# Performance work log

Hardware: AMD Instinct MI355X
Metric: run time of the kernel (lower is better)

## Reference

```python
import jax, jax.numpy as jnp
import numpy as np

LN_EPS = 1e-5   # nn.LayerNorm default eps
EPS = 1e-3      # norm epsilon in module

B, R, S, C, CO, OUT = 1, 256, 128, 256, 32, 128  # res, seq, c_m, outer_channel, output_channel


def setup_inputs() -> dict:
    key = jax.random.key(0)
    ks = jax.random.split(key, 6)
    act = jax.random.normal(ks[0], (B, R, S, C), jnp.float32)
    mask = jnp.ones((B, S, R), jnp.float32)
    ln_gamma = jnp.ones((C,), jnp.float32)
    ln_beta = jnp.zeros((C,), jnp.float32)
    w_left = jax.random.normal(ks[1], (CO, C), jnp.float32) * (1.0 / np.sqrt(C))
    b_left = jnp.zeros((CO,), jnp.float32)
    w_right = jax.random.normal(ks[2], (CO, C), jnp.float32) * (1.0 / np.sqrt(C))
    b_right = jnp.zeros((CO,), jnp.float32)
    w_o = jax.random.normal(ks[3], (OUT, CO * CO), jnp.float32) * (1.0 / np.sqrt(CO * CO))
    b_o = jnp.zeros((OUT,), jnp.float32)
    return {"act": act, "mask": mask, "ln_gamma": ln_gamma, "ln_beta": ln_beta,
            "w_left": w_left, "b_left": b_left, "w_right": w_right, "b_right": b_right,
            "w_o": w_o, "b_o": b_o}


def reference(act, mask, ln_gamma, ln_beta, w_left, b_left, w_right, b_right, w_o, b_o):
    # act: [B, R(res), S(seq), C]; mask: [B, S, R]
    x = jnp.swapaxes(act, -3, -2)                     # permute_final_dims (1,0,2) -> [B, S, R, C]
    mu = x.mean(-1, keepdims=True)
    var = x.var(-1, keepdims=True)
    xn = (x - mu) * jax.lax.rsqrt(var + LN_EPS) * ln_gamma + ln_beta
    m = mask[..., None]                               # [B, S, R, 1]
    left = m * (xn @ w_left.T + b_left)               # [B, S, R, CO]
    right = m * (xn @ w_right.T + b_right)            # [B, S, R, CO]
    # outer product mean over seq dim: out[b,i,j,c,d] = sum_s left[b,s,i,c] * right[b,s,j,d]
    op = jnp.einsum('bsic,bsjd->bijcd', left, right)  # [B, R, R, CO, CO]
    op = op.reshape(op.shape[:3] + (CO * CO,))        # flatten_final_dims(.., 2)
    out = op @ w_o.T + b_o                            # [B, R, R, OUT]
    norm = jnp.einsum('bsi,bsj->bij', mask, mask)[..., None]  # [B, R, R, 1]
    return out / (EPS + norm)
```

## Files before the change

### kernel.cpp

```cpp
#include <hip/hip_runtime.h>
#include <hip/hip_bf16.h>
#include <stdint.h>

#define R_ 256
#define S_ 128
#define C_ 256
#define CO_ 32
#define OUT_ 128
#define LN_EPS 1e-5f
#define EPS_ 1e-3f

typedef __attribute__((ext_vector_type(8))) short bf16x8;
typedef __attribute__((ext_vector_type(4))) float f32x4;

static __device__ __forceinline__ unsigned short f2bf(float f) {
  union { float f; uint32_t u; } cv; cv.f = f;
  uint32_t u = cv.u;
  uint32_t r = (u + 0x7FFFu + ((u >> 16) & 1u)) >> 16;
  return (unsigned short)r;
}

__global__ void k_prep_w(const float* wl, const float* wr, const float* gamma,
                         const float* beta, const float* bl, const float* br,
                         unsigned short* wcat, float* g1, float* g0, float* bcat) {
  int co = blockIdx.x;
  int c = threadIdx.x;
  const float* src = (co < 32) ? (wl + co * C_) : (wr + (co - 32) * C_);
  float w = src[c], g = gamma[c], bt = beta[c];
  float wg = w * g;
  wcat[co * C_ + c] = f2bf(wg);
  __shared__ float red1[256], red0[256];
  red1[c] = wg; red0[c] = w * bt;
  __syncthreads();
  for (int off = 128; off > 0; off >>= 1) {
    if (c < off) { red1[c] += red1[c + off]; red0[c] += red0[c + off]; }
    __syncthreads();
  }
  if (c == 0) {
    g1[co] = red1[0];
    g0[co] = red0[0];
    bcat[co] = (co < 32) ? bl[co] : br[co - 32];
  }
}

__global__ void k_cast_wo(const float* wo, unsigned short* wob) {
  int t = blockIdx.x * 256 + threadIdx.x;
  float4 v = ((const float4*)wo)[t];
  ushort4 o;
  o.x = f2bf(v.x); o.y = f2bf(v.y); o.z = f2bf(v.z); o.w = f2bf(v.w);
  ((ushort4*)wob)[t] = o;
}

__global__ void k_norm(const float* mask, float* invn) {
  int i = blockIdx.x, j = threadIdx.x;
  float a = 0.f;
  for (int s = 0; s < S_; ++s) a += mask[s * R_ + i] * mask[s * R_ + j];
  invn[i * R_ + j] = 1.0f / (EPS_ + a);
}

#define AP 264
__global__ __launch_bounds__(256) void k_proj(
    const float* act, const float* mask, const unsigned short* wcat,
    const float* g1v, const float* g0v, const float* bcv,
    unsigned short* leftg, unsigned short* rightg) {
  __shared__ unsigned short a_bf[S_ * AP];
  __shared__ unsigned short w_l[64 * AP];
  __shared__ float mu_s[S_], rs_s[S_], mk_s[S_];
  __shared__ float g1s[64], g0s[64], bcs[64];
  int tid = threadIdx.x;
  int r = blockIdx.x;

  const float4* actv = (const float4*)(act + (size_t)r * (S_ * C_));
  for (int it = 0; it < 32; ++it) {
    int f = tid + it * 256;
    int s = f >> 6;
    int c4 = (f & 63) * 4;
    float4 v = actv[f];
    ushort4 o;
    o.x = f2bf(v.x); o.y = f2bf(v.y); o.z = f2bf(v.z); o.w = f2bf(v.w);
    *(ushort4*)&a_bf[s * AP + c4] = o;
  }
  const uint4* wsrc = (const uint4*)wcat;
  for (int it = 0; it < 8; ++it) {
    int f = tid + it * 256;
    int co = f >> 5, ch = f & 31;
    *(uint4*)&w_l[co * AP + ch * 8] = wsrc[f];
  }
  if (tid < 128) mk_s[tid] = mask[tid * R_ + r];
  if (tid < 64) { g1s[tid] = g1v[tid]; g0s[tid] = g0v[tid]; bcs[tid] = bcv[tid]; }
  __syncthreads();

  if (tid < 128) {
    float sum = 0.f, sq = 0.f;
    for (int i = 0; i < 32; ++i) {
      uint4 v = *(const uint4*)&a_bf[tid * AP + i * 8];
      uint32_t ws_[4] = {v.x, v.y, v.z, v.w};
#pragma unroll
      for (int q = 0; q < 4; ++q) {
        union { uint32_t u; float f; } lo, hi;
        lo.u = ws_[q] << 16;
        hi.u = ws_[q] & 0xFFFF0000u;
        sum += lo.f + hi.f;
        sq += lo.f * lo.f + hi.f * hi.f;
      }
    }
    float mu = sum * (1.0f / C_);
    float var = sq * (1.0f / C_) - mu * mu;
    mu_s[tid] = mu;
    rs_s[tid] = rsqrtf(var + LN_EPS);
  }
  __syncthreads();

  int lane = tid & 63, wid = tid >> 6;
  int l15 = lane & 15, l4 = lane >> 4;
  f32x4 acc[2][4];
#pragma unroll
  for (int a = 0; a < 2; ++a)
#pragma unroll
    for (int b = 0; b < 4; ++b) acc[a][b] = (f32x4){0.f, 0.f, 0.f, 0.f};
  for (int ks = 0; ks < 8; ++ks) {
    bf16x8 af[2], bfr[4];
#pragma unroll
    for (int mf = 0; mf < 2; ++mf) {
      int row = wid * 32 + mf * 16 + l15;
      af[mf] = *(const bf16x8*)&a_bf[row * AP + ks * 32 + l4 * 8];
    }
#pragma unroll
    for (int nf = 0; nf < 4; ++nf) {
      int row = nf * 16 + l15;
      bfr[nf] = *(const bf16x8*)&w_l[row * AP + ks * 32 + l4 * 8];
    }
#pragma unroll
    for (int mf = 0; mf < 2; ++mf)
#pragma unroll
      for (int nf = 0; nf < 4; ++nf)
        acc[mf][nf] = __builtin_amdgcn_mfma_f32_16x16x32_bf16(af[mf], bfr[nf], acc[mf][nf], 0, 0, 0);
  }
  __syncthreads();

  unsigned short* trans = w_l;
#pragma unroll
  for (int mf = 0; mf < 2; ++mf) {
#pragma unroll
    for (int nf = 0; nf < 4; ++nf) {
      int co = nf * 16 + l15;
      float G1 = g1s[co], G0 = g0s[co], BC = bcs[co];
#pragma unroll
      for (int reg = 0; reg < 4; ++reg) {
        int s = wid * 32 + mf * 16 + l4 * 4 + reg;
        float v = rs_s[s] * acc[mf][nf][reg] - mu_s[s] * rs_s[s] * G1 + G0 + BC;
        v *= mk_s[s];
        trans[co * 136 + s] = f2bf(v);
      }
    }
  }
  __syncthreads();

  uint4* lg = (uint4*)leftg;
  uint4* rg = (uint4*)rightg;
  for (int it = 0; it < 4; ++it) {
    int idx = tid + it * 256;
    int row = idx >> 4, ch = idx & 15;
    uint4 val = *(const uint4*)&trans[row * 136 + ch * 8];
    if (row < 32) lg[((size_t)r * 32 + row) * 16 + ch] = val;
    else          rg[((size_t)r * 32 + (row - 32)) * 16 + ch] = val;
  }
}

#define SROW 136
#define OPROW 1032
__global__ __launch_bounds__(512, 2) void k_main(
    const unsigned short* __restrict__ leftg, const unsigned short* __restrict__ rightg,
    const unsigned short* __restrict__ wob, const float* __restrict__ bo,
    const float* __restrict__ invn, float* __restrict__ out) {
  __shared__ __align__(16) unsigned char sm[2 * 256 * 272];
  unsigned short* sa = (unsigned short*)sm;
  unsigned short* sb = (unsigned short*)(sm + 256 * 272);
  unsigned short* opb = (unsigned short*)sm;
  int tid = threadIdx.x;
  int bi = blockIdx.x >> 5, bj = blockIdx.x & 31;

  const uint4* lsrc = (const uint4*)leftg + (size_t)bi * 256 * 16;
  const uint4* rsrc = (const uint4*)rightg + (size_t)bj * 256 * 16;
  for (int it = 0; it < 8; ++it) {
    int idx = tid + it * 512;
    int row = idx >> 4, ch = idx & 15;
    *(uint4*)&sa[row * SROW + ch * 8] = lsrc[idx];
    *(uint4*)&sb[row * SROW + ch * 8] = rsrc[idx];
  }
  __syncthreads();

  int lane = tid & 63, w = tid >> 6;
  int l15 = lane & 15, l4 = lane >> 4;

  int wm = w >> 2, wn = w & 3;
  f32x4 acc[8][4];
#pragma unroll
  for (int a = 0; a < 8; ++a)
#pragma unroll
    for (int b = 0; b < 4; ++b) acc[a][b] = (f32x4){0.f, 0.f, 0.f, 0.f};
  for (int ks = 0; ks < 4; ++ks) {
    bf16x8 af[8], bfr[4];
#pragma unroll
    for (int mf = 0; mf < 8; ++mf)
      af[mf] = *(const bf16x8*)&sa[(wm * 128 + mf * 16 + l15) * SROW + ks * 32 + l4 * 8];
#pragma unroll
    for (int nf = 0; nf < 4; ++nf)
      bfr[nf] = *(const bf16x8*)&sb[(wn * 64 + nf * 16 + l15) * SROW + ks * 32 + l4 * 8];
#pragma unroll
    for (int mf = 0; mf < 8; ++mf)
#pragma unroll
      for (int nf = 0; nf < 4; ++nf)
        acc[mf][nf] = __builtin_amdgcn_mfma_f32_16x16x32_bf16(af[mf], bfr[nf], acc[mf][nf], 0, 0, 0);
  }
  __syncthreads();

#pragma unroll
  for (int mf = 0; mf < 8; ++mf) {
    int mbase = wm * 128 + mf * 16 + l4 * 4;
#pragma unroll
    for (int nf = 0; nf < 4; ++nf) {
      int n = wn * 64 + nf * 16 + l15;
      int j = n >> 5, d = n & 31;
#pragma unroll
      for (int reg = 0; reg < 4; ++reg) {
        int m = mbase + reg;
        int i = m >> 5, c = m & 31;
        opb[(i * 8 + j) * OPROW + c * 32 + d] = f2bf(acc[mf][nf][reg]);
      }
    }
  }
  __syncthreads();

  int o = w * 16 + l15;
  f32x4 acc2[4];
#pragma unroll
  for (int a = 0; a < 4; ++a) acc2[a] = (f32x4){0.f, 0.f, 0.f, 0.f};
  const uint4* wrow = (const uint4*)(wob + (size_t)o * 1024);
  uint4 bnext = wrow[l4];
  for (int ks2 = 0; ks2 < 32; ++ks2) {
    uint4 bcur = bnext;
    if (ks2 < 31) bnext = wrow[(ks2 + 1) * 4 + l4];
    bf16x8 b2 = *(const bf16x8*)&bcur;
    bf16x8 a2[4];
#pragma unroll
    for (int mf = 0; mf < 4; ++mf)
      a2[mf] = *(const bf16x8*)&opb[(mf * 16 + l15) * OPROW + ks2 * 32 + l4 * 8];
#pragma unroll
    for (int mf = 0; mf < 4; ++mf)
      acc2[mf] = __builtin_amdgcn_mfma_f32_16x16x32_bf16(a2[mf], b2, acc2[mf], 0, 0, 0);
  }

  float bov = bo[o];
#pragma unroll
  for (int mf = 0; mf < 4; ++mf) {
#pragma unroll
    for (int reg = 0; reg < 4; ++reg) {
      int p = mf * 16 + l4 * 4 + reg;
      int gi = bi * 8 + (p >> 3), gj = bj * 8 + (p & 7);
      float v = (acc2[mf][reg] + bov) * invn[gi * R_ + gj];
      out[((size_t)(gi * R_ + gj)) * OUT_ + o] = v;
    }
  }
}

extern "C" void kernel_launch(void* const* d_in, const int* in_sizes, int n_in,
                              void* d_out, int out_size, void* d_ws, size_t ws_size,
                              hipStream_t stream) {
  (void)in_sizes; (void)n_in; (void)out_size; (void)ws_size;
  const float* act   = (const float*)d_in[0];
  const float* mask  = (const float*)d_in[1];
  const float* gamma = (const float*)d_in[2];
  const float* beta  = (const float*)d_in[3];
  const float* wl    = (const float*)d_in[4];
  const float* bl    = (const float*)d_in[5];
  const float* wr    = (const float*)d_in[6];
  const float* br    = (const float*)d_in[7];
  const float* wo    = (const float*)d_in[8];
  const float* bo    = (const float*)d_in[9];
  float* out = (float*)d_out;
  unsigned char* ws = (unsigned char*)d_ws;
  unsigned short* leftg  = (unsigned short*)(ws + 0);
  unsigned short* rightg = (unsigned short*)(ws + 2097152);
  unsigned short* wob    = (unsigned short*)(ws + 4194304);
  float* invn            = (float*)(ws + 4456448);
  unsigned short* wcat   = (unsigned short*)(ws + 4718592);
  float* g1              = (float*)(ws + 4751360);
  float* g0              = (float*)(ws + 4751616);
  float* bcat            = (float*)(ws + 4751872);

  hipLaunchKernelGGL(k_prep_w, dim3(64), dim3(256), 0, stream,
                     wl, wr, gamma, beta, bl, br, wcat, g1, g0, bcat);
  hipLaunchKernelGGL(k_cast_wo, dim3(128), dim3(256), 0, stream, wo, wob);
  hipLaunchKernelGGL(k_norm, dim3(256), dim3(256), 0, stream, mask, invn);
  hipLaunchKernelGGL(k_proj, dim3(256), dim3(256), 0, stream,
                     act, mask, wcat, g1, g0, bcat, leftg, rightg);
  hipLaunchKernelGGL(k_main, dim3(1024), dim3(512), 0, stream,
                     leftg, rightg, wob, bo, invn, out);
}
```

Baseline: 173.1 us.

## Merge prep kernels, split projection over seq halves, swizzle LDS and split-K output GEMM

Fuses the three weight/norm prep kernels into one launch and pre-permutes w_o into an MFMA-friendly tiled layout. The projection kernel now runs two blocks per residue, each covering half the sequence, and computes LayerNorm statistics in fp32 with wave shuffles while loading. The main kernel loads left/right tiles straight into XOR-swizzled LDS with global_load_lds and writes the outer-product buffer swizzled to avoid bank conflicts. The output GEMM is split over K across two wave groups and reduced through LDS. These changes target launch overhead, LDS bank conflicts and load latency, at the cost of an extra reduction pass and more complex indexing.

```diff
diff --git a/kernel.cpp b/kernel.cpp
--- a/kernel.cpp
+++ b/kernel.cpp
@@ -12,6 +12,8 @@
 
 typedef __attribute__((ext_vector_type(8))) short bf16x8;
 typedef __attribute__((ext_vector_type(4))) float f32x4;
+typedef __attribute__((address_space(1))) const unsigned int GAS;
+typedef __attribute__((address_space(3))) unsigned int LAS;
 
 static __device__ __forceinline__ unsigned short f2bf(float f) {
   union { float f; uint32_t u; } cv; cv.f = f;
@@ -20,178 +22,162 @@
   return (unsigned short)r;
 }
 
-__global__ void k_prep_w(const float* wl, const float* wr, const float* gamma,
-                         const float* beta, const float* bl, const float* br,
-                         unsigned short* wcat, float* g1, float* g0, float* bcat) {
-  int co = blockIdx.x;
-  int c = threadIdx.x;
-  const float* src = (co < 32) ? (wl + co * C_) : (wr + (co - 32) * C_);
-  float w = src[c], g = gamma[c], bt = beta[c];
-  float wg = w * g;
-  wcat[co * C_ + c] = f2bf(wg);
-  __shared__ float red1[256], red0[256];
-  red1[c] = wg; red0[c] = w * bt;
-  __syncthreads();
-  for (int off = 128; off > 0; off >>= 1) {
-    if (c < off) { red1[c] += red1[c + off]; red0[c] += red0[c + off]; }
+__global__ __launch_bounds__(256) void k_prep(
+    const float* wl, const float* wr, const float* gamma, const float* beta,
+    const float* bl, const float* br, const float* wo, const float* mask,
+    unsigned short* wcat, float* g1, float* g0, float* bcat,
+    unsigned short* wob2, float* invn) {
+  int bid = blockIdx.x, tid = threadIdx.x;
+  if (bid < 64) {
+    int co = bid, c = tid;
+    const float* src = (co < 32) ? (wl + co * C_) : (wr + (co - 32) * C_);
+    float w = src[c], g = gamma[c], bt = beta[c];
+    float wg = w * g;
+    wcat[co * C_ + c] = f2bf(wg);
+    __shared__ float red1[256], red0[256];
+    red1[c] = wg; red0[c] = w * bt;
     __syncthreads();
-  }
-  if (c == 0) {
-    g1[co] = red1[0];
-    g0[co] = red0[0];
-    bcat[co] = (co < 32) ? bl[co] : br[co - 32];
-  }
-}
-
-__global__ void k_cast_wo(const float* wo, unsigned short* wob) {
-  int t = blockIdx.x * 256 + threadIdx.x;
-  float4 v = ((const float4*)wo)[t];
-  ushort4 o;
-  o.x = f2bf(v.x); o.y = f2bf(v.y); o.z = f2bf(v.z); o.w = f2bf(v.w);
-  ((ushort4*)wob)[t] = o;
-}
-
-__global__ void k_norm(const float* mask, float* invn) {
-  int i = blockIdx.x, j = threadIdx.x;
-  float a = 0.f;
-  for (int s = 0; s < S_; ++s) a += mask[s * R_ + i] * mask[s * R_ + j];
-  invn[i * R_ + j] = 1.0f / (EPS_ + a);
-}
-
-#define AP 264
-__global__ __launch_bounds__(256) void k_proj(
-    const float* act, const float* mask, const unsigned short* wcat,
-    const float* g1v, const float* g0v, const float* bcv,
-    unsigned short* leftg, unsigned short* rightg) {
-  __shared__ unsigned short a_bf[S_ * AP];
-  __shared__ unsigned short w_l[64 * AP];
-  __shared__ float mu_s[S_], rs_s[S_], mk_s[S_];
+    for (int off = 128; off > 0; off >>= 1) {
+      if (c < off) { red1[c] += red1[c + off]; red0[c] += red0[c + off]; }
+      __syncthreads();
+    }
+    if (c == 0) {
+      g1[co] = red1[0]; g0[co] = red0[0];
+      bcat[co] = (co < 32) ? bl[co] : br[co - 32];
+    }
+  } else if (bid < 192) {
+    int o = bid - 64;
+    float4 v = ((const float4*)wo)[o * 256 + tid];
+    float vv[4] = {v.x, v.y, v.z, v.w};
+#pragma unroll
+    for (int e = 0; e < 4; ++e) {
+      int kk = tid * 4 + e;
+      int kk2 = (kk & 31) * 32 + (kk >> 5);
+      wob2[(kk2 >> 3) * 1024 + o * 8 + (kk2 & 7)] = f2bf(vv[e]);
+    }
+  } else {
+    int i = bid - 192, j = tid;
+    float a = 0.f;
+    for (int s = 0; s < S_; ++s) a += mask[s * R_ + i] * mask[s * R_ + j];
+    invn[i * R_ + j] = 1.0f / (EPS_ + a);
+  }
+}
+
+#define AP2 264
+__global__ __launch_bounds__(256, 2) void k_proj(
+    const float* __restrict__ act, const float* __restrict__ mask,
+    const unsigned short* __restrict__ wcat,
+    const float* __restrict__ g1v, const float* __restrict__ g0v,
+    const float* __restrict__ bcv,
+    unsigned short* __restrict__ leftg, unsigned short* __restrict__ rightg) {
+  __shared__ __align__(16) unsigned short a_bf[64 * AP2];
+  __shared__ __align__(16) unsigned short w_l[64 * AP2];
+  __shared__ __align__(16) unsigned short trans[64 * 72];
+  __shared__ float mu_s[64], rs_s[64], mk_s[64];
   __shared__ float g1s[64], g0s[64], bcs[64];
   int tid = threadIdx.x;
-  int r = blockIdx.x;
-
-  const float4* actv = (const float4*)(act + (size_t)r * (S_ * C_));
-  for (int it = 0; it < 32; ++it) {
-    int f = tid + it * 256;
-    int s = f >> 6;
-    int c4 = (f & 63) * 4;
-    float4 v = actv[f];
+  int lane = tid & 63, w = tid >> 6;
+  int r = blockIdx.x >> 1;
+  int sh = (blockIdx.x & 1) * 64;
+
+  const float4* actv = (const float4*)act;
+  for (int it = 0; it < 16; ++it) {
+    int s = w + it * 4;
+    float4 v = actv[(size_t)r * 8192 + (size_t)(sh + s) * 64 + lane];
+    float ls = v.x + v.y + v.z + v.w;
+    float lq = v.x * v.x + v.y * v.y + v.z * v.z + v.w * v.w;
+#pragma unroll
+    for (int off = 32; off > 0; off >>= 1) {
+      ls += __shfl_xor(ls, off);
+      lq += __shfl_xor(lq, off);
+    }
+    if (lane == 0) {
+      float mu = ls * (1.0f / 256.0f);
+      float var = lq * (1.0f / 256.0f) - mu * mu;
+      mu_s[s] = mu;
+      rs_s[s] = rsqrtf(var + LN_EPS);
+    }
     ushort4 o;
     o.x = f2bf(v.x); o.y = f2bf(v.y); o.z = f2bf(v.z); o.w = f2bf(v.w);
-    *(ushort4*)&a_bf[s * AP + c4] = o;
+    *(ushort4*)&a_bf[s * AP2 + lane * 4] = o;
   }
   const uint4* wsrc = (const uint4*)wcat;
   for (int it = 0; it < 8; ++it) {
     int f = tid + it * 256;
     int co = f >> 5, ch = f & 31;
-    *(uint4*)&w_l[co * AP + ch * 8] = wsrc[f];
-  }
-  if (tid < 128) mk_s[tid] = mask[tid * R_ + r];
-  if (tid < 64) { g1s[tid] = g1v[tid]; g0s[tid] = g0v[tid]; bcs[tid] = bcv[tid]; }
-  __syncthreads();
-
-  if (tid < 128) {
-    float sum = 0.f, sq = 0.f;
-    for (int i = 0; i < 32; ++i) {
-      uint4 v = *(const uint4*)&a_bf[tid * AP + i * 8];
-      uint32_t ws_[4] = {v.x, v.y, v.z, v.w};
-#pragma unroll
-      for (int q = 0; q < 4; ++q) {
-        union { uint32_t u; float f; } lo, hi;
-        lo.u = ws_[q] << 16;
-        hi.u = ws_[q] & 0xFFFF0000u;
-        sum += lo.f + hi.f;
-        sq += lo.f * lo.f + hi.f * hi.f;
-      }
-    }
-    float mu = sum * (1.0f / C_);
-    float var = sq * (1.0f / C_) - mu * mu;
-    mu_s[tid] = mu;
-    rs_s[tid] = rsqrtf(var + LN_EPS);
-  }
-  __syncthreads();
-
-  int lane = tid & 63, wid = tid >> 6;
+    *(uint4*)&w_l[co * AP2 + ch * 8] = wsrc[f];
+  }
+  if (tid < 64) {
+    mk_s[tid] = mask[(size_t)(sh + tid) * R_ + r];
+    g1s[tid] = g1v[tid]; g0s[tid] = g0v[tid]; bcs[tid] = bcv[tid];
+  }
+  __syncthreads();
+
   int l15 = lane & 15, l4 = lane >> 4;
-  f32x4 acc[2][4];
-#pragma unroll
-  for (int a = 0; a < 2; ++a)
-#pragma unroll
-    for (int b = 0; b < 4; ++b) acc[a][b] = (f32x4){0.f, 0.f, 0.f, 0.f};
+  f32x4 acc[4];
+#pragma unroll
+  for (int b = 0; b < 4; ++b) acc[b] = (f32x4){0.f, 0.f, 0.f, 0.f};
   for (int ks = 0; ks < 8; ++ks) {
-    bf16x8 af[2], bfr[4];
-#pragma unroll
-    for (int mf = 0; mf < 2; ++mf) {
-      int row = wid * 32 + mf * 16 + l15;
-      af[mf] = *(const bf16x8*)&a_bf[row * AP + ks * 32 + l4 * 8];
-    }
+    bf16x8 af = *(const bf16x8*)&a_bf[(w * 16 + l15) * AP2 + ks * 32 + l4 * 8];
 #pragma unroll
     for (int nf = 0; nf < 4; ++nf) {
-      int row = nf * 16 + l15;
-      bfr[nf] = *(const bf16x8*)&w_l[row * AP + ks * 32 + l4 * 8];
-    }
-#pragma unroll
-    for (int mf = 0; mf < 2; ++mf)
-#pragma unroll
-      for (int nf = 0; nf < 4; ++nf)
-        acc[mf][nf] = __builtin_amdgcn_mfma_f32_16x16x32_bf16(af[mf], bfr[nf], acc[mf][nf], 0, 0, 0);
-  }
-  __syncthreads();
-
-  unsigned short* trans = w_l;
-#pragma unroll
-  for (int mf = 0; mf < 2; ++mf) {
-#pragma unroll
-    for (int nf = 0; nf < 4; ++nf) {
-      int co = nf * 16 + l15;
-      float G1 = g1s[co], G0 = g0s[co], BC = bcs[co];
-#pragma unroll
-      for (int reg = 0; reg < 4; ++reg) {
-        int s = wid * 32 + mf * 16 + l4 * 4 + reg;
-        float v = rs_s[s] * acc[mf][nf][reg] - mu_s[s] * rs_s[s] * G1 + G0 + BC;
-        v *= mk_s[s];
-        trans[co * 136 + s] = f2bf(v);
-      }
-    }
-  }
-  __syncthreads();
-
-  uint4* lg = (uint4*)leftg;
-  uint4* rg = (uint4*)rightg;
-  for (int it = 0; it < 4; ++it) {
-    int idx = tid + it * 256;
-    int row = idx >> 4, ch = idx & 15;
-    uint4 val = *(const uint4*)&trans[row * 136 + ch * 8];
-    if (row < 32) lg[((size_t)r * 32 + row) * 16 + ch] = val;
-    else          rg[((size_t)r * 32 + (row - 32)) * 16 + ch] = val;
-  }
-}
-
-#define SROW 136
-#define OPROW 1032
+      bf16x8 bfr = *(const bf16x8*)&w_l[(nf * 16 + l15) * AP2 + ks * 32 + l4 * 8];
+      acc[nf] = __builtin_amdgcn_mfma_f32_16x16x32_bf16(af, bfr, acc[nf], 0, 0, 0);
+    }
+  }
+#pragma unroll
+  for (int nf = 0; nf < 4; ++nf) {
+    int co = nf * 16 + l15;
+    float G1 = g1s[co], G0 = g0s[co], BC = bcs[co];
+#pragma unroll
+    for (int reg = 0; reg < 4; ++reg) {
+      int s = w * 16 + l4 * 4 + reg;
+      float v = rs_s[s] * acc[nf][reg] - mu_s[s] * rs_s[s] * G1 + G0 + BC;
+      v *= mk_s[s];
+      trans[co * 72 + s] = f2bf(v);
+    }
+  }
+  __syncthreads();
+
+  for (int it2 = 0; it2 < 2; ++it2) {
+    int idx = tid + it2 * 256;
+    int row = idx >> 3, ch = idx & 7;
+    uint4 val = *(const uint4*)&trans[row * 72 + ch * 8];
+    if (row < 32)
+      ((uint4*)leftg)[((size_t)(r * 32 + row)) * 16 + (sh >> 3) + ch] = val;
+    else
+      ((uint4*)rightg)[((size_t)(r * 32 + row - 32)) * 16 + (sh >> 3) + ch] = val;
+  }
+}
+
 __global__ __launch_bounds__(512, 2) void k_main(
     const unsigned short* __restrict__ leftg, const unsigned short* __restrict__ rightg,
-    const unsigned short* __restrict__ wob, const float* __restrict__ bo,
+    const unsigned short* __restrict__ wob2, const float* __restrict__ bo,
     const float* __restrict__ invn, float* __restrict__ out) {
-  __shared__ __align__(16) unsigned char sm[2 * 256 * 272];
-  unsigned short* sa = (unsigned short*)sm;
-  unsigned short* sb = (unsigned short*)(sm + 256 * 272);
-  unsigned short* opb = (unsigned short*)sm;
+  __shared__ __align__(16) unsigned char smem[131072];
+  unsigned char* opbytes = smem;
+  unsigned short* opu16 = (unsigned short*)smem;
+  float* redf = (float*)smem;
   int tid = threadIdx.x;
-  int bi = blockIdx.x >> 5, bj = blockIdx.x & 31;
-
-  const uint4* lsrc = (const uint4*)leftg + (size_t)bi * 256 * 16;
-  const uint4* rsrc = (const uint4*)rightg + (size_t)bj * 256 * 16;
-  for (int it = 0; it < 8; ++it) {
-    int idx = tid + it * 512;
-    int row = idx >> 4, ch = idx & 15;
-    *(uint4*)&sa[row * SROW + ch * 8] = lsrc[idx];
-    *(uint4*)&sb[row * SROW + ch * 8] = rsrc[idx];
-  }
-  __syncthreads();
-
   int lane = tid & 63, w = tid >> 6;
   int l15 = lane & 15, l4 = lane >> 4;
+  int bi = blockIdx.x >> 5, bj = blockIdx.x & 31;
+
+  {
+    const unsigned char* gA = (const unsigned char*)leftg + (size_t)bi * 65536;
+    const unsigned char* gB = (const unsigned char*)rightg + (size_t)bj * 65536;
+#pragma unroll
+    for (int k = 0; k < 8; ++k) {
+      int rowbase = w * 32 + k * 4;
+      int row = rowbase + (lane >> 4);
+      int ch = (lane & 15) ^ (row & 7);
+      __builtin_amdgcn_global_load_lds((GAS*)(gA + row * 256 + ch * 16),
+                                       (LAS*)&smem[rowbase * 256], 16, 0, 0);
+      __builtin_amdgcn_global_load_lds((GAS*)(gB + row * 256 + ch * 16),
+                                       (LAS*)&smem[65536 + rowbase * 256], 16, 0, 0);
+    }
+  }
+  __syncthreads();
 
   int wm = w >> 2, wn = w & 3;
   f32x4 acc[8][4];
@@ -202,11 +188,17 @@
   for (int ks = 0; ks < 4; ++ks) {
     bf16x8 af[8], bfr[4];
 #pragma unroll
-    for (int mf = 0; mf < 8; ++mf)
-      af[mf] = *(const bf16x8*)&sa[(wm * 128 + mf * 16 + l15) * SROW + ks * 32 + l4 * 8];
-#pragma unroll
-    for (int nf = 0; nf < 4; ++nf)
-      bfr[nf] = *(const bf16x8*)&sb[(wn * 64 + nf * 16 + l15) * SROW + ks * 32 + l4 * 8];
+    for (int mf = 0; mf < 8; ++mf) {
+      int row = wm * 128 + mf * 16 + l15;
+      int ch = (ks * 4 + l4) ^ (row & 7);
+      af[mf] = *(const bf16x8*)&smem[row * 256 + ch * 16];
+    }
+#pragma unroll
+    for (int nf = 0; nf < 4; ++nf) {
+      int row = wn * 64 + nf * 16 + l15;
+      int ch = (ks * 4 + l4) ^ (row & 7);
+      bfr[nf] = *(const bf16x8*)&smem[65536 + row * 256 + ch * 16];
+    }
 #pragma unroll
     for (int mf = 0; mf < 8; ++mf)
 #pragma unroll
@@ -217,49 +209,79 @@
 
 #pragma unroll
   for (int mf = 0; mf < 8; ++mf) {
-    int mbase = wm * 128 + mf * 16 + l4 * 4;
 #pragma unroll
     for (int nf = 0; nf < 4; ++nf) {
-      int n = wn * 64 + nf * 16 + l15;
-      int j = n >> 5, d = n & 31;
-#pragma unroll
-      for (int reg = 0; reg < 4; ++reg) {
-        int m = mbase + reg;
-        int i = m >> 5, c = m & 31;
-        opb[(i * 8 + j) * OPROW + c * 32 + d] = f2bf(acc[mf][nf][reg]);
+      int p = (wm * 4 + (mf >> 1)) * 8 + wn * 2 + (nf >> 1);
+      int d = ((nf & 1) << 4) + l15;
+      int c0 = ((mf & 1) << 4) + l4 * 4;
+      int baddr = p * 2048 + ((d * 64 + c0 * 2) ^ ((p & 7) << 4));
+      uint32_t h0 = f2bf(acc[mf][nf][0]), h1 = f2bf(acc[mf][nf][1]);
+      uint32_t h2 = f2bf(acc[mf][nf][2]), h3 = f2bf(acc[mf][nf][3]);
+      uint2 pk; pk.x = h0 | (h1 << 16); pk.y = h2 | (h3 << 16);
+      *(uint2*)&opbytes[baddr] = pk;
+    }
+  }
+  __syncthreads();
+
+  int kh = w >> 2, wn2 = w & 3;
+  f32x4 acc2[4][2];
+#pragma unroll
+  for (int a = 0; a < 4; ++a) { acc2[a][0] = (f32x4){0,0,0,0}; acc2[a][1] = (f32x4){0,0,0,0}; }
+  {
+    const uint4* wv = (const uint4*)wob2;
+    int ks0 = kh * 16;
+#pragma unroll 2
+    for (int ks2 = ks0; ks2 < ks0 + 16; ++ks2) {
+      uint4 b0r = wv[(ks2 * 4 + l4) * 128 + wn2 * 32 + l15];
+      uint4 b1r = wv[(ks2 * 4 + l4) * 128 + wn2 * 32 + 16 + l15];
+      bf16x8 b0 = *(const bf16x8*)&b0r;
+      bf16x8 b1 = *(const bf16x8*)&b1r;
+      bf16x8 a2[4];
+#pragma unroll
+      for (int mf = 0; mf < 4; ++mf) {
+        int p = mf * 16 + l15;
+        int ch = (ks2 * 4 + l4) ^ (p & 7);
+        a2[mf] = *(const bf16x8*)&opu16[p * 1024 + ch * 8];
       }
-    }
-  }
-  __syncthreads();
-
-  int o = w * 16 + l15;
-  f32x4 acc2[4];
-#pragma unroll
-  for (int a = 0; a < 4; ++a) acc2[a] = (f32x4){0.f, 0.f, 0.f, 0.f};
-  const uint4* wrow = (const uint4*)(wob + (size_t)o * 1024);
-  uint4 bnext = wrow[l4];
-  for (int ks2 = 0; ks2 < 32; ++ks2) {
-    uint4 bcur = bnext;
-    if (ks2 < 31) bnext = wrow[(ks2 + 1) * 4 + l4];
-    bf16x8 b2 = *(const bf16x8*)&bcur;
-    bf16x8 a2[4];
+#pragma unroll
+      for (int mf = 0; mf < 4; ++mf) {
+        acc2[mf][0] = __builtin_amdgcn_mfma_f32_16x16x32_bf16(a2[mf], b0, acc2[mf][0], 0, 0, 0);
+        acc2[mf][1] = __builtin_amdgcn_mfma_f32_16x16x32_bf16(a2[mf], b1, acc2[mf][1], 0, 0, 0);
+      }
+    }
+  }
+  __syncthreads();
+
+  if (kh == 1) {
 #pragma unroll
     for (int mf = 0; mf < 4; ++mf)
-      a2[mf] = *(const bf16x8*)&opb[(mf * 16 + l15) * OPROW + ks2 * 32 + l4 * 8];
+#pragma unroll
+      for (int n2 = 0; n2 < 2; ++n2)
+        *(f32x4*)&redf[((w - 4) * 64 + lane) * 36 + (mf * 2 + n2) * 4] = acc2[mf][n2];
+  }
+  __syncthreads();
+  if (kh == 0) {
 #pragma unroll
     for (int mf = 0; mf < 4; ++mf)
-      acc2[mf] = __builtin_amdgcn_mfma_f32_16x16x32_bf16(a2[mf], b2, acc2[mf], 0, 0, 0);
-  }
-
-  float bov = bo[o];
-#pragma unroll
-  for (int mf = 0; mf < 4; ++mf) {
-#pragma unroll
-    for (int reg = 0; reg < 4; ++reg) {
-      int p = mf * 16 + l4 * 4 + reg;
-      int gi = bi * 8 + (p >> 3), gj = bj * 8 + (p & 7);
-      float v = (acc2[mf][reg] + bov) * invn[gi * R_ + gj];
-      out[((size_t)(gi * R_ + gj)) * OUT_ + o] = v;
+#pragma unroll
+      for (int n2 = 0; n2 < 2; ++n2) {
+        f32x4 pv = *(const f32x4*)&redf[(w * 64 + lane) * 36 + (mf * 2 + n2) * 4];
+        acc2[mf][n2] += pv;
+      }
+#pragma unroll
+    for (int n2 = 0; n2 < 2; ++n2) {
+      int o = wn2 * 32 + n2 * 16 + l15;
+      float bov = bo[o];
+#pragma unroll
+      for (int mf = 0; mf < 4; ++mf) {
+#pragma unroll
+        for (int reg = 0; reg < 4; ++reg) {
+          int p = mf * 16 + l4 * 4 + reg;
+          int gi = bi * 8 + (p >> 3), gj = bj * 8 + (p & 7);
+          float v = (acc2[mf][n2][reg] + bov) * invn[gi * R_ + gj];
+          out[((size_t)(gi * R_ + gj)) * OUT_ + o] = v;
+        }
+      }
     }
   }
 }
@@ -282,19 +304,18 @@
   unsigned char* ws = (unsigned char*)d_ws;
   unsigned short* leftg  = (unsigned short*)(ws + 0);
   unsigned short* rightg = (unsigned short*)(ws + 2097152);
-  unsigned short* wob    = (unsigned short*)(ws + 4194304);
+  unsigned short* wob2   = (unsigned short*)(ws + 4194304);
   float* invn            = (float*)(ws + 4456448);
   unsigned short* wcat   = (unsigned short*)(ws + 4718592);
   float* g1              = (float*)(ws + 4751360);
   float* g0              = (float*)(ws + 4751616);
   float* bcat            = (float*)(ws + 4751872);
 
-  hipLaunchKernelGGL(k_prep_w, dim3(64), dim3(256), 0, stream,
-                     wl, wr, gamma, beta, bl, br, wcat, g1, g0, bcat);
-  hipLaunchKernelGGL(k_cast_wo, dim3(128), dim3(256), 0, stream, wo, wob);
-  hipLaunchKernelGGL(k_norm, dim3(256), dim3(256), 0, stream, mask, invn);
-  hipLaunchKernelGGL(k_proj, dim3(256), dim3(256), 0, stream,
+  hipLaunchKernelGGL(k_prep, dim3(448), dim3(256), 0, stream,
+                     wl, wr, gamma, beta, bl, br, wo, mask,
+                     wcat, g1, g0, bcat, wob2, invn);
+  hipLaunchKernelGGL(k_proj, dim3(512), dim3(256), 0, stream,
                      act, mask, wcat, g1, g0, bcat, leftg, rightg);
   hipLaunchKernelGGL(k_main, dim3(1024), dim3(512), 0, stream,
-                     leftg, rightg, wob, bo, invn, out);
-}
+                     leftg, rightg, wob2, bo, invn, out);
+}
```

After: 160.1 us. 1.08x faster.
